# Performance work log

Measured on AMD Instinct MI355X. Metric: run time of the kernel, lower is better.

Reference implementation:

```python
import jax, jax.numpy as jnp
import numpy as np

N_CVS = 4096
FEAT = 128
BATCH = 8192
K = 15
EPSILON = 0.9
E_MIN = 0.9 ** 10


def setup_inputs() -> dict:
    key = jax.random.key(0)
    k1, k2, k3 = jax.random.split(key, 3)
    x = jax.random.normal(k1, (BATCH, FEAT), dtype=jnp.float32)
    labels = jax.random.randint(k2, (BATCH,), 0, N_CVS, dtype=jnp.int64 if jax.config.jax_enable_x64 else jnp.int32)
    cvs = jax.random.normal(k3, (N_CVS, FEAT), dtype=jnp.float32)
    # module state buffers: identity-initialized edge / connectedness matrices
    edges = jnp.eye(N_CVS, dtype=jnp.float32)
    cv_connectedness = jnp.eye(N_CVS, dtype=jnp.float32)
    return {"x": x, "cvs": cvs, "edges": edges, "cv_connectedness": cv_connectedness, "labels": labels}


def reference(x, cvs, edges, cv_connectedness, labels):
    B = x.shape[0]
    N = cvs.shape[0]
    # squared pairwise distances (same ordering as cdist; x_cvs = cdist**2)
    d2 = (jnp.sum(x * x, axis=1)[:, None]
          + jnp.sum(cvs * cvs, axis=1)[None, :]
          - 2.0 * (x @ cvs.T))
    d2 = jnp.maximum(d2, 0.0)  # [B, N]

    # k nearest codevectors per sample (smallest distance first)
    _, knn = jax.lax.top_k(-d2, K)        # [B, K]
    closest = knn[:, 0]                    # [B]

    # visits per codevector (Counter over closest)
    visits = jnp.zeros((N,), dtype=jnp.float32).at[closest].add(1.0)
    # encounters[i, j] = visits[i]
    encounters = jnp.broadcast_to(visits[:, None], (N, N))

    # closest_cv_encounters[closest[i], knn[i, k]] += 1
    rows = jnp.repeat(closest, K)
    cols = knn.reshape(-1)
    cce = jnp.zeros((N, N), dtype=jnp.float32).at[rows, cols].add(1.0)

    existence = cce > 0
    enc = jnp.maximum(encounters - cce, 0.0)

    # edge update (state): refresh visited edges, exponentially decay others
    edges_new = jnp.maximum(edges, existence.astype(edges.dtype))
    edges_new = edges_new * (EPSILON ** enc)
    edges_new = jnp.where(edges_new < E_MIN, 0.0, edges_new)

    # margin loss
    d_pos = jnp.sum((x - cvs[labels]) ** 2, axis=1)                  # [B]
    neigh_mask = (edges_new > 0) & (cv_connectedness < 1)            # [N, N]
    d_neg = d2 * neigh_mask[labels].astype(d2.dtype)                 # [B, N]
    e_neg = jnp.exp(-0.001 * d_neg) * (d_neg > 0)
    w = e_neg / jnp.sum(e_neg, axis=1, keepdims=True)
    w = jnp.where(jnp.isnan(w), 0.0, w)
    w = jax.lax.stop_gradient(w)
    mu = d_pos - jnp.sum(w * d_neg, axis=1)
    loss = jnp.sum(jnp.maximum(mu, 0.0)) / B
    return loss
```

## Files before the change

### kernel.cpp

```cpp
#include <hip/hip_runtime.h>
#include <math.h>

#define N_CVS   4096
#define FEAT    128
#define BATCH   8192
#define KNN_K   15
#define E_MIN_F 0.34867844f

typedef __attribute__((ext_vector_type(8))) short bf16x8;
typedef __attribute__((ext_vector_type(4))) float f32x4;
typedef __attribute__((ext_vector_type(4))) unsigned int u32x4;

__global__ void cvtnorm_kernel(const float* __restrict__ x, const float* __restrict__ cvs,
                               unsigned short* __restrict__ xb, unsigned short* __restrict__ cb,
                               float* __restrict__ x2, float* __restrict__ c2) {
    size_t tid = (size_t)blockIdx.x * 256 + threadIdx.x;
    size_t f = tid * 8;
    const float* src; unsigned short* dst; float* ndst; size_t row;
    if (f < (size_t)BATCH * FEAT) { src = x + f; dst = xb + f; row = f >> 7; ndst = x2 + row; }
    else {
        size_t g = f - (size_t)BATCH * FEAT;
        src = cvs + g; dst = cb + g; row = g >> 7; ndst = c2 + row;
    }
    float4 v0 = ((const float4*)src)[0];
    float4 v1 = ((const float4*)src)[1];
    float vv[8] = {v0.x, v0.y, v0.z, v0.w, v1.x, v1.y, v1.z, v1.w};
    bf16x8 o;
    float s = 0.f;
    #pragma unroll
    for (int i = 0; i < 8; ++i) {
        unsigned u = __float_as_uint(vv[i]);
        o[i] = (short)((u + 0x7fffu + ((u >> 16) & 1u)) >> 16);
        s += vv[i] * vv[i];
    }
    *(bf16x8*)dst = o;
    #pragma unroll
    for (int off = 1; off < 16; off <<= 1) s += __shfl_xor(s, off, 64);
    if ((threadIdx.x & 15) == 0) *ndst = s;
}

#define LROW 272
__global__ __launch_bounds__(256) void mfma_d2_kernel(
        const unsigned short* __restrict__ xb, const unsigned short* __restrict__ cb,
        const float* __restrict__ x2g, const float* __restrict__ c2g,
        float* __restrict__ d2) {
    __shared__ __align__(16) char lds[2 * 128 * LROW];
    char* Al = lds;
    char* Bl = lds + 128 * LROW;
    const int bi = blockIdx.y * 128;
    const int bj = blockIdx.x * 128;
    const int t  = threadIdx.x;

    #pragma unroll
    for (int i = 0; i < 8; ++i) {
        int f = t + i * 256;
        int row = f >> 4, g = f & 15;
        ulonglong2 va = *(const ulonglong2*)((const char*)(xb + (size_t)(bi + row) * FEAT) + g * 16);
        *(ulonglong2*)(Al + row * LROW + g * 16) = va;
        ulonglong2 vb = *(const ulonglong2*)((const char*)(cb + (size_t)(bj + row) * FEAT) + g * 16);
        *(ulonglong2*)(Bl + row * LROW + g * 16) = vb;
    }
    __syncthreads();

    const int lane = t & 63;
    const int wave = t >> 6;
    const int wr = (wave >> 1) * 64;
    const int wc = (wave & 1) * 64;
    const int l15 = lane & 15, quad = lane >> 4;

    f32x4 acc[4][4];
    #pragma unroll
    for (int i = 0; i < 4; ++i)
        #pragma unroll
        for (int j = 0; j < 4; ++j)
            acc[i][j] = (f32x4){0.f, 0.f, 0.f, 0.f};

    #pragma unroll
    for (int ks = 0; ks < 4; ++ks) {
        bf16x8 a[4], b[4];
        #pragma unroll
        for (int s = 0; s < 4; ++s) {
            a[s] = *(const bf16x8*)(Al + (wr + s * 16 + l15) * LROW + ks * 64 + quad * 16);
            b[s] = *(const bf16x8*)(Bl + (wc + s * 16 + l15) * LROW + ks * 64 + quad * 16);
        }
        #pragma unroll
        for (int si = 0; si < 4; ++si)
            #pragma unroll
            for (int sj = 0; sj < 4; ++sj)
                acc[si][sj] = __builtin_amdgcn_mfma_f32_16x16x32_bf16(a[si], b[sj], acc[si][sj], 0, 0, 0);
    }

    #pragma unroll
    for (int si = 0; si < 4; ++si) {
        #pragma unroll
        for (int r = 0; r < 4; ++r) {
            int m = bi + wr + si * 16 + quad * 4 + r;
            float xv = x2g[m];
            float* orow = d2 + (size_t)m * N_CVS + bj + wc;
            #pragma unroll
            for (int sj = 0; sj < 4; ++sj) {
                int nloc = sj * 16 + l15;
                float v = xv + c2g[bj + wc + nloc] - 2.0f * acc[si][sj][r];
                orow[nloc] = fmaxf(v, 0.0f);
            }
        }
    }
}

__global__ __launch_bounds__(256, 3) void topk_kernel(const float* __restrict__ d2,
                                                      int* __restrict__ knn) {
    __shared__ unsigned long long cand[4][64];
    const int wv   = threadIdx.x >> 6;
    const int wid  = blockIdx.x * 4 + wv;
    const int lane = threadIdx.x & 63;
    const float* row = d2 + (size_t)wid * N_CVS;

    float4 v[16];
    #pragma unroll
    for (int i = 0; i < 16; ++i)
        v[i] = *(const float4*)(row + lane * 4 + i * 256);

    float mn = fminf(fminf(v[0].x, v[0].y), fminf(v[0].z, v[0].w));
    #pragma unroll
    for (int i = 1; i < 16; ++i)
        mn = fminf(mn, fminf(fminf(v[i].x, v[i].y), fminf(v[i].z, v[i].w)));

    float s = mn;
    #pragma unroll
    for (int k = 2; k <= 64; k <<= 1) {
        #pragma unroll
        for (int j = k >> 1; j > 0; j >>= 1) {
            float o = __shfl_xor(s, j, 64);
            bool lower = ((lane & j) == 0);
            bool asc   = ((lane & k) == 0);
            float lo = fminf(s, o), hi = fmaxf(s, o);
            s = (lower == asc) ? lo : hi;
        }
    }
    float T = __shfl(s, 15, 64);

    unsigned long long* cbuf = cand[wv];
    int base = 0;
    #pragma unroll
    for (int i = 0; i < 16; ++i) {
        float vv[4] = {v[i].x, v[i].y, v[i].z, v[i].w};
        #pragma unroll
        for (int c = 0; c < 4; ++c) {
            bool p = (vv[c] <= T);
            unsigned long long mask = __ballot(p);
            if (p) {
                int pos = base + __popcll(mask & ((1ULL << lane) - 1ULL));
                if (pos < 64)
                    cbuf[pos] = ((unsigned long long)__float_as_uint(vv[c]) << 32)
                              | (unsigned)(lane * 4 + i * 256 + c);
            }
            base += __popcll(mask);
        }
    }
    __builtin_amdgcn_wave_barrier();

    int* outp = knn + wid * KNN_K;
    if (base <= 64) {
        unsigned long long key = (lane < base) ? cbuf[lane] : ~0ULL;
        for (int r = 0; r < KNN_K; ++r) {
            unsigned long long m = key;
            #pragma unroll
            for (int off = 32; off > 0; off >>= 1) {
                unsigned long long o = __shfl_xor(m, off, 64);
                m = (o < m) ? o : m;
            }
            if (lane == 0) outp[r] = (int)(unsigned)(m & 0xffffffffu);
            if (key == m) key = ~0ULL;
        }
    } else {
        unsigned long long heap[15];
        #pragma unroll
        for (int k = 0; k < 15; ++k) heap[k] = ~0ULL;
        for (int i = 0; i < 16; ++i) {
            int j0 = lane * 4 + i * 256;
            float4 f4 = *(const float4*)(row + j0);
            float vv[4] = {f4.x, f4.y, f4.z, f4.w};
            #pragma unroll
            for (int c = 0; c < 4; ++c) {
                unsigned long long key =
                    ((unsigned long long)__float_as_uint(vv[c]) << 32) | (unsigned)(j0 + c);
                if (key < heap[14]) {
                    heap[14] = key;
                    #pragma unroll
                    for (int k = 14; k > 0; --k) {
                        unsigned long long a = heap[k-1], b = heap[k];
                        bool sw = b < a;
                        heap[k-1] = sw ? b : a;
                        heap[k]   = sw ? a : b;
                    }
                }
            }
        }
        for (int r = 0; r < KNN_K; ++r) {
            unsigned long long cd = heap[0];
            unsigned long long m = cd;
            #pragma unroll
            for (int off = 32; off > 0; off >>= 1) {
                unsigned long long o = __shfl_xor(m, off, 64);
                m = (o < m) ? o : m;
            }
            if (lane == 0) outp[r] = (int)(unsigned)(m & 0xffffffffu);
            if (cd == m) {
                #pragma unroll
                for (int k = 0; k < 14; ++k) heap[k] = heap[k+1];
                heap[14] = ~0ULL;
            }
        }
    }
}

__global__ void scatter_kernel(const int* __restrict__ knn, int* __restrict__ visits,
                               unsigned int* __restrict__ cce8) {
    int b = blockIdx.x * 256 + threadIdx.x;
    const int* kr = knn + b * KNN_K;
    int closest = kr[0];
    atomicAdd(&visits[closest], 1);
    size_t base = (size_t)closest * N_CVS;
    #pragma unroll
    for (int k = 0; k < KNN_K; ++k) {
        size_t idx = base + kr[k];
        atomicAdd((int*)&cce8[idx >> 2], 1 << ((idx & 3) * 8));
    }
}

__global__ __launch_bounds__(256) void bits_kernel(
        const unsigned int* __restrict__ cce8, const int* __restrict__ visits,
        const float* __restrict__ edges, const float* __restrict__ conn,
        unsigned short* __restrict__ bits16) {
    const int row = blockIdx.x;
    const int t   = threadIdx.x;
    const int vis = visits[row];
    size_t eb = (size_t)row * N_CVS + t * 16;
    f32x4 e[4];
    #pragma unroll
    for (int q = 0; q < 4; ++q) e[q] = ((const f32x4*)(edges + eb))[q];
    u32x4 cw = ((const u32x4*)(cce8 + (size_t)row * 1024))[t];

    unsigned pre = 0;
    #pragma unroll
    for (int q = 0; q < 4; ++q) {
        #pragma unroll
        for (int s = 0; s < 4; ++s) {
            int cc = (cw[q] >> (s * 8)) & 0xff;
            float ev = e[q][s];
            float ex = (cc > 0) ? fmaxf(ev, 1.0f) : ev;
            bool p;
            if (ex == 1.0f) {
                p = (vis - cc) <= 9;
            } else if (ex > 0.0f) {
                float enc = fmaxf((float)(vis - cc), 0.0f);
                p = ex * powf(0.9f, enc) >= E_MIN_F;
            } else {
                p = false;
            }
            pre |= (unsigned)p << (q * 4 + s);
        }
    }
    unsigned m = 0;
    #pragma unroll
    for (int q = 0; q < 4; ++q) {
        unsigned pn = (pre >> (q * 4)) & 0xfu;
        if (pn) {
            f32x4 cv = ((const f32x4*)(conn + eb))[q];
            #pragma unroll
            for (int s = 0; s < 4; ++s)
                if (((pn >> s) & 1u) && (cv[s] < 1.0f)) m |= 1u << (q * 4 + s);
        }
    }
    bits16[(size_t)row * 256 + t] = (unsigned short)m;
}

__global__ void loss_kernel(const float* __restrict__ d2,
                            const unsigned long long* __restrict__ bits,
                            const int* __restrict__ labels, float* __restrict__ partial) {
    int wid  = blockIdx.x * 4 + (threadIdx.x >> 6);
    int lane = threadIdx.x & 63;
    int l = labels[wid];
    const unsigned long long* rb = bits + (size_t)l * 64;
    const float* row = d2 + (size_t)wid * N_CVS;
    float se = 0.f, sed = 0.f;
    unsigned long long w = rb[lane];
    while (w) {
        int c = __builtin_ctzll(w);
        w &= w - 1;
        int j = lane * 64 + c;
        float d = row[j];
        if (d > 0.f) {
            float ee = __expf(-0.001f * d);
            se += ee; sed += ee * d;
        }
    }
    #pragma unroll
    for (int off = 32; off > 0; off >>= 1) {
        se  += __shfl_xor(se,  off, 64);
        sed += __shfl_xor(sed, off, 64);
    }
    if (lane == 0) {
        float dpos = row[l];
        float wsum = se > 0.f ? sed / se : 0.f;
        float mu = dpos - wsum;
        partial[wid] = (mu > 0.f) ? mu : 0.f;
    }
}

__global__ void reduce_kernel(const float* __restrict__ partial, float* __restrict__ out) {
    int t = threadIdx.x;
    float s = 0.f;
    #pragma unroll
    for (int i = 0; i < BATCH / 256; ++i) s += partial[t + i * 256];
    #pragma unroll
    for (int off = 32; off > 0; off >>= 1) s += __shfl_xor(s, off, 64);
    __shared__ float wsum[4];
    if ((t & 63) == 0) wsum[t >> 6] = s;
    __syncthreads();
    if (t == 0) out[0] = (wsum[0] + wsum[1] + wsum[2] + wsum[3]) * (1.0f / BATCH);
}

extern "C" void kernel_launch(void* const* d_in, const int* in_sizes, int n_in,
                              void* d_out, int out_size, void* d_ws, size_t ws_size,
                              hipStream_t stream) {
    const float* x      = (const float*)d_in[0];
    const float* cvs    = (const float*)d_in[1];
    const float* edges  = (const float*)d_in[2];
    const float* conn   = (const float*)d_in[3];
    const int*   labels = (const int*)d_in[4];

    char* p = (char*)d_ws;
    float* d2 = (float*)p;                  p += (size_t)BATCH * N_CVS * 4;
    int* knn  = (int*)p;                    p += (size_t)BATCH * KNN_K * 4;
    int* visits = (int*)p;                  p += (size_t)N_CVS * 4;
    unsigned int* cce8 = (unsigned int*)p;  p += (size_t)N_CVS * N_CVS;
    unsigned long long* bits = (unsigned long long*)p;
                                            p += (size_t)N_CVS * 64 * 8;
    float* x2 = (float*)p;                  p += (size_t)BATCH * 4;
    float* c2 = (float*)p;                  p += (size_t)N_CVS * 4;
    unsigned short* xb = (unsigned short*)p; p += (size_t)BATCH * FEAT * 2;
    unsigned short* cb = (unsigned short*)p; p += (size_t)N_CVS * FEAT * 2;
    float* partial = (float*)p;             p += (size_t)BATCH * 4;

    hipMemsetAsync(visits, 0, (size_t)N_CVS * 4 + (size_t)N_CVS * N_CVS, stream);

    cvtnorm_kernel<<<(BATCH + N_CVS) * FEAT / 8 / 256, 256, 0, stream>>>(x, cvs, xb, cb, x2, c2);
    mfma_d2_kernel<<<dim3(N_CVS / 128, BATCH / 128), 256, 0, stream>>>(xb, cb, x2, c2, d2);
    topk_kernel   <<<BATCH / 4, 256, 0, stream>>>(d2, knn);
    scatter_kernel<<<BATCH / 256, 256, 0, stream>>>(knn, visits, cce8);
    bits_kernel   <<<N_CVS, 256, 0, stream>>>(
                      cce8, visits, edges, conn, (unsigned short*)bits);
    loss_kernel   <<<BATCH / 4, 256, 0, stream>>>(d2, bits, labels, partial);
    reduce_kernel <<<1, 256, 0, stream>>>(partial, (float*)d_out);
}
```

Baseline: 223.8 us.

## Compute per-chunk row minima in GEMM epilogue to prune top-k row scans

The distance GEMM epilogue now records, for each row, the minimum over each 128-column chunk and writes it to a small rowmin buffer. The top-k kernel sorts these 32 chunk minima and takes the 15th smallest as its threshold. It then loads only the chunks whose minimum is at or below that threshold, instead of reading the whole 4096-wide row. This replaces a full read of the d2 matrix in top-k with a mostly sparse read, at the cost of LDS atomics and shuffles in the GEMM epilogue plus divergent per-chunk loads.

```diff
diff --git a/kernel.cpp b/kernel.cpp
--- a/kernel.cpp
+++ b/kernel.cpp
@@ -43,14 +43,16 @@
 __global__ __launch_bounds__(256) void mfma_d2_kernel(
         const unsigned short* __restrict__ xb, const unsigned short* __restrict__ cb,
         const float* __restrict__ x2g, const float* __restrict__ c2g,
-        float* __restrict__ d2) {
+        float* __restrict__ d2, float* __restrict__ rowmin) {
     __shared__ __align__(16) char lds[2 * 128 * LROW];
+    __shared__ unsigned int rmin[128];
     char* Al = lds;
     char* Bl = lds + 128 * LROW;
     const int bi = blockIdx.y * 128;
     const int bj = blockIdx.x * 128;
     const int t  = threadIdx.x;
 
+    if (t < 128) rmin[t] = 0xffffffffu;
     #pragma unroll
     for (int i = 0; i < 8; ++i) {
         int f = t + i * 256;
@@ -94,38 +96,42 @@
     for (int si = 0; si < 4; ++si) {
         #pragma unroll
         for (int r = 0; r < 4; ++r) {
-            int m = bi + wr + si * 16 + quad * 4 + r;
+            int mloc = wr + si * 16 + quad * 4 + r;
+            int m = bi + mloc;
             float xv = x2g[m];
             float* orow = d2 + (size_t)m * N_CVS + bj + wc;
+            float mn = INFINITY;
             #pragma unroll
             for (int sj = 0; sj < 4; ++sj) {
                 int nloc = sj * 16 + l15;
                 float v = xv + c2g[bj + wc + nloc] - 2.0f * acc[si][sj][r];
-                orow[nloc] = fmaxf(v, 0.0f);
-            }
-        }
-    }
-}
-
-__global__ __launch_bounds__(256, 3) void topk_kernel(const float* __restrict__ d2,
-                                                      int* __restrict__ knn) {
+                v = fmaxf(v, 0.0f);
+                mn = fminf(mn, v);
+                orow[nloc] = v;
+            }
+            #pragma unroll
+            for (int off = 1; off < 16; off <<= 1)
+                mn = fminf(mn, __shfl_xor(mn, off, 64));
+            if (l15 == 0)
+                atomicMin(&rmin[mloc], __float_as_uint(mn));
+        }
+    }
+    __syncthreads();
+    if (t < 128)
+        rowmin[(size_t)(bi + t) * 32 + blockIdx.x] = __uint_as_float(rmin[t]);
+}
+
+__global__ __launch_bounds__(256) void topk_kernel(const float* __restrict__ d2,
+                                                   const float* __restrict__ rowmin,
+                                                   int* __restrict__ knn) {
     __shared__ unsigned long long cand[4][64];
     const int wv   = threadIdx.x >> 6;
     const int wid  = blockIdx.x * 4 + wv;
     const int lane = threadIdx.x & 63;
     const float* row = d2 + (size_t)wid * N_CVS;
 
-    float4 v[16];
-    #pragma unroll
-    for (int i = 0; i < 16; ++i)
-        v[i] = *(const float4*)(row + lane * 4 + i * 256);
-
-    float mn = fminf(fminf(v[0].x, v[0].y), fminf(v[0].z, v[0].w));
-    #pragma unroll
-    for (int i = 1; i < 16; ++i)
-        mn = fminf(mn, fminf(fminf(v[i].x, v[i].y), fminf(v[i].z, v[i].w)));
-
-    float s = mn;
+    float cm = rowmin[(size_t)wid * 32 + (lane & 31)];
+    float s = (lane < 32) ? cm : INFINITY;
     #pragma unroll
     for (int k = 2; k <= 64; k <<= 1) {
         #pragma unroll
@@ -137,24 +143,27 @@
             s = (lower == asc) ? lo : hi;
         }
     }
-    float T = __shfl(s, 15, 64);
+    float T = __shfl(s, 14, 64);
 
     unsigned long long* cbuf = cand[wv];
     int base = 0;
-    #pragma unroll
-    for (int i = 0; i < 16; ++i) {
-        float vv[4] = {v[i].x, v[i].y, v[i].z, v[i].w};
-        #pragma unroll
-        for (int c = 0; c < 4; ++c) {
-            bool p = (vv[c] <= T);
-            unsigned long long mask = __ballot(p);
-            if (p) {
-                int pos = base + __popcll(mask & ((1ULL << lane) - 1ULL));
-                if (pos < 64)
-                    cbuf[pos] = ((unsigned long long)__float_as_uint(vv[c]) << 32)
-                              | (unsigned)(lane * 4 + i * 256 + c);
-            }
-            base += __popcll(mask);
+    for (int c = 0; c < 32; ++c) {
+        float mc = __shfl(cm, c, 64);
+        if (mc <= T) {
+            float2 v2 = *(const float2*)(row + c * 128 + lane * 2);
+            float vv[2] = {v2.x, v2.y};
+            #pragma unroll
+            for (int h = 0; h < 2; ++h) {
+                bool p = (vv[h] <= T);
+                unsigned long long mask = __ballot(p);
+                if (p) {
+                    int pos = base + __popcll(mask & ((1ULL << lane) - 1ULL));
+                    if (pos < 64)
+                        cbuf[pos] = ((unsigned long long)__float_as_uint(vv[h]) << 32)
+                                  | (unsigned)(c * 128 + lane * 2 + h);
+                }
+                base += __popcll(mask);
+            }
         }
     }
     __builtin_amdgcn_wave_barrier();
@@ -342,12 +351,13 @@
     unsigned short* xb = (unsigned short*)p; p += (size_t)BATCH * FEAT * 2;
     unsigned short* cb = (unsigned short*)p; p += (size_t)N_CVS * FEAT * 2;
     float* partial = (float*)p;             p += (size_t)BATCH * 4;
+    float* rowmin = (float*)p;              p += (size_t)BATCH * 32 * 4;
 
     hipMemsetAsync(visits, 0, (size_t)N_CVS * 4 + (size_t)N_CVS * N_CVS, stream);
 
     cvtnorm_kernel<<<(BATCH + N_CVS) * FEAT / 8 / 256, 256, 0, stream>>>(x, cvs, xb, cb, x2, c2);
-    mfma_d2_kernel<<<dim3(N_CVS / 128, BATCH / 128), 256, 0, stream>>>(xb, cb, x2, c2, d2);
-    topk_kernel   <<<BATCH / 4, 256, 0, stream>>>(d2, knn);
+    mfma_d2_kernel<<<dim3(N_CVS / 128, BATCH / 128), 256, 0, stream>>>(xb, cb, x2, c2, d2, rowmin);
+    topk_kernel   <<<BATCH / 4, 256, 0, stream>>>(d2, rowmin, knn);
     scatter_kernel<<<BATCH / 256, 256, 0, stream>>>(knn, visits, cce8);
     bits_kernel   <<<N_CVS, 256, 0, stream>>>(
                       cce8, visits, edges, conn, (unsigned short*)bits);
```

After: 239.3 us. +6.9%, slower.
